# Optimization experiments

Hardware: AMD Instinct MI355X
Metric: run time of the kernel (lower is better)

## Reference

```python
import jax, jax.numpy as jnp
import numpy as np

EMBED = 2048
HEADS = 16
HEAD_DIM = EMBED // HEADS
CHUNK = 128
BASE = 10000.0
EPS = 1e-6


def setup_inputs() -> dict:
    key = jax.random.key(0)
    ks = jax.random.split(key, 8)
    b, n, d = 2, 2048, EMBED
    std = 0.02
    return {
        "x": jax.random.normal(ks[0], (b, n, d), jnp.float32),
        "Wq": jax.random.normal(ks[1], (d, d), jnp.float32) * std,
        "Wk": jax.random.normal(ks[2], (d, d), jnp.float32) * std,
        "Wv": jax.random.normal(ks[3], (d, d), jnp.float32) * std,
        "Wo": jax.random.normal(ks[4], (d, d), jnp.float32) * std,
        "Wg1": jax.random.normal(ks[5], (d, HEAD_DIM), jnp.float32) * std,
        "Wg2": jax.random.normal(ks[6], (HEAD_DIM, d), jnp.float32) * std,
        "norm_weight": jnp.ones((d,), jnp.float32),
    }


def _alibi_log_decay(h):
    # lightning attention 'constant' decay: per-head ALiBi slope, log_lambda = -slope
    slopes = 2.0 ** (-8.0 * (jnp.arange(h, dtype=jnp.float32) + 1.0) / h)
    return -slopes  # [h]


def _lrpe_rotate(x):
    # RoPE-like rotation on head_dim (half-split), offset=0
    b, n, h, d = x.shape
    half = d // 2
    theta = BASE ** (-2.0 * jnp.arange(half, dtype=jnp.float32) / d)  # [half]
    ang = jnp.arange(n, dtype=jnp.float32)[:, None] * theta[None, :]  # [n, half]
    cos = jnp.cos(ang)[None, :, None, :]
    sin = jnp.sin(ang)[None, :, None, :]
    x1, x2 = x[..., :half], x[..., half:]
    return jnp.concatenate([x1 * cos - x2 * sin, x1 * sin + x2 * cos], axis=-1)


def _lightning_attn(q, k, v, log_lam):
    # chunk-recurrent linear attention with per-head exponential decay
    b, n, h, d = q.shape
    C = CHUNK
    nc = n // C
    qc = q.reshape(b, nc, C, h, d).transpose(1, 0, 2, 3, 4)  # [nc,b,C,h,d]
    kc = k.reshape(b, nc, C, h, d).transpose(1, 0, 2, 3, 4)
    vc = v.reshape(b, nc, C, h, d).transpose(1, 0, 2, 3, 4)
    i = jnp.arange(C, dtype=jnp.float32)
    diff = i[:, None] - i[None, :]  # [C,C]
    # intra-chunk decay mask D[h,t,s] = lambda_h^(t-s) for t>=s else 0
    D = jnp.where(diff[None] >= 0, jnp.exp(log_lam[:, None, None] * diff[None]), 0.0)
    decay_q = jnp.exp(log_lam[None, :] * (i[:, None] + 1.0))    # [C,h]
    decay_k = jnp.exp(log_lam[None, :] * (C - 1.0 - i[:, None]))  # [C,h]
    lam_C = jnp.exp(log_lam * C)  # [h]

    def step(S, qkv):
        qi, ki, vi = qkv  # [b,C,h,d]
        scores = jnp.einsum('bthd,bshd->bhts', qi, ki) * D[None]
        o_intra = jnp.einsum('bhts,bshd->bthd', scores, vi)
        o_inter = jnp.einsum('bthd,bhde->bthe', qi * decay_q[None, :, :, None], S)
        S_new = lam_C[None, :, None, None] * S + jnp.einsum(
            'bshd,bshe->bhde', ki * decay_k[None, :, :, None], vi)
        return S_new, o_intra + o_inter

    S0 = jnp.zeros((b, h, d, d), q.dtype)
    _, o = jax.lax.scan(step, S0, (qc, kc, vc))  # o: [nc,b,C,h,d]
    return o.transpose(1, 0, 2, 3, 4).reshape(b, n, h, d)


def _gated_group_rmsnorm(o, gate, weight):
    # gate_pos='pre', gate_act='sigmoid', num_groups=HEADS
    b, n, d = o.shape
    x = o * jax.nn.sigmoid(gate)
    xg = x.reshape(b, n, HEADS, HEAD_DIM)
    ms = jnp.mean(xg * xg, axis=-1, keepdims=True)
    xg = xg * jax.lax.rsqrt(ms + EPS)
    return xg.reshape(b, n, d) * weight


def reference(x, Wq, Wk, Wv, Wo, Wg1, Wg2, norm_weight):
    b, n, d = x.shape
    q = (x @ Wq).reshape(b, n, HEADS, HEAD_DIM)
    k = (x @ Wk).reshape(b, n, HEADS, HEAD_DIM)
    v = (x @ Wv).reshape(b, n, HEADS, HEAD_DIM)
    q = jax.nn.silu(q)
    k = jax.nn.silu(k)
    q = _lrpe_rotate(q)
    k = _lrpe_rotate(k)
    log_lam = _alibi_log_decay(HEADS)
    o = _lightning_attn(q, k, v, log_lam).reshape(b, n, d)
    gate = (x @ Wg1) @ Wg2
    o = _gated_group_rmsnorm(o, gate, norm_weight)
    return o @ Wo
```

## Files before the change

kernel.cpp:

```cpp
#include <hip/hip_runtime.h>


#define DEV __device__ __forceinline__
typedef unsigned short u16;
typedef __bf16 bf16x8 __attribute__((ext_vector_type(8)));
typedef float f32x4 __attribute__((ext_vector_type(4)));
typedef u16 u16x8 __attribute__((ext_vector_type(8)));

DEV u16 f2bf(float f) {
  unsigned u = __builtin_bit_cast(unsigned, f);
  u += 0x7fffu + ((u >> 16) & 1u);
  return (u16)(u >> 16);
}
DEV float bf2f(u16 h) {
  unsigned u = ((unsigned)h) << 16;
  return __builtin_bit_cast(float, u);
}
DEV void async16(const u16* g, u16* l) {
  __builtin_amdgcn_global_load_lds(
      (const __attribute__((address_space(1))) unsigned int*)g,
      (__attribute__((address_space(3))) unsigned int*)l, 16, 0, 0);
}

__global__ void convert_f32_bf16(const float* __restrict__ in, u16* __restrict__ out, long n) {
  long i = ((long)blockIdx.x * blockDim.x + threadIdx.x) * 4;
  if (i >= n) return;
  float4 v = *(const float4*)(in + i);
  ushort4 p;
  p.x = f2bf(v.x); p.y = f2bf(v.y); p.z = f2bf(v.z); p.w = f2bf(v.w);
  *(ushort4*)(out + i) = p;
}

__global__ void transpose_all(const float* __restrict__ Wq, const float* __restrict__ Wk,
                              const float* __restrict__ Wv, const float* __restrict__ Wo,
                              const float* __restrict__ Wg1, const float* __restrict__ Wg2,
                              u16* __restrict__ wtqkv, u16* __restrict__ wot,
                              u16* __restrict__ wg1t, u16* __restrict__ wg2t) {
  __shared__ float t[32][33];
  int id = blockIdx.x;
  const float* in; u16* out; int K, N, bx, by;
  if (id < 12288) {
    int w = id >> 12, tt = id & 4095;
    in = (w == 0) ? Wq : (w == 1) ? Wk : Wv;
    out = wtqkv + (long)w * 2048 * 2048;
    K = 2048; N = 2048; bx = tt & 63; by = tt >> 6;
  } else if (id < 16384) {
    int tt = id - 12288;
    in = Wo; out = wot; K = 2048; N = 2048; bx = tt & 63; by = tt >> 6;
  } else if (id < 16640) {
    int tt = id - 16384;
    in = Wg1; out = wg1t; K = 2048; N = 128; bx = tt & 3; by = tt >> 2;
  } else {
    int tt = id - 16640;
    in = Wg2; out = wg2t; K = 128; N = 2048; bx = tt & 63; by = tt >> 6;
  }
  int c = threadIdx.x & 31, r0 = threadIdx.x >> 5;
  for (int r = r0; r < 32; r += 8)
    t[r][c] = in[(long)(by * 32 + r) * N + bx * 32 + c];
  __syncthreads();
  for (int r = r0; r < 32; r += 8)
    out[(long)(bx * 32 + r) * K + by * 32 + c] = f2bf(t[c][r]);
}

template <typename OutT>
__global__ __launch_bounds__(256, 2) void gemm_bt(
    const u16* __restrict__ A, const u16* __restrict__ B, OutT* __restrict__ C,
    int M, int N, int K, int lda, int ldb, int ldc,
    int nc, long sA1, long sA2, long sB1, long sB2, long sC1, long sC2) {
  __shared__ u16 sA[128 * 32], sB[128 * 32];
  {
    int z = blockIdx.z, z1 = z / nc, z2 = z % nc;
    A += z1 * sA1 + z2 * sA2;
    B += z1 * sB1 + z2 * sB2;
    C += z1 * sC1 + z2 * sC2;
  }
  const int tid = threadIdx.x, lane = tid & 63, wid = tid >> 6;
  const int bm = blockIdx.y * 128, bn = blockIdx.x * 128;
  const int ch0 = wid * 2, ch1 = ch0 + 1;
  const int lr = lane >> 2;
  const int ak = (((lane & 3) - ((lane >> 3) & 3)) & 3) * 8;
  const int ar0 = ch0 * 16 + lr, ar1 = ch1 * 16 + lr;
  const u16* gA0 = A + (long)(bm + ar0) * lda + ak;
  const u16* gA1 = A + (long)(bm + ar1) * lda + ak;
  const u16* gB0 = B + (long)(bn + ar0) * ldb + ak;
  const u16* gB1 = B + (long)(bn + ar1) * ldb + ak;
  u16* lA0 = sA + ch0 * 512; u16* lA1 = sA + ch1 * 512;
  u16* lB0 = sB + ch0 * 512; u16* lB1 = sB + ch1 * 512;
  const int wm = (wid & 1) * 64, wn = (wid >> 1) * 64;
  const int fm = lane & 15, kq = lane >> 4;
  const int qs = ((kq + (fm >> 1)) & 3) * 8;
  const int aoff = (wm >> 4) * 512 + fm * 32 + qs;
  const int boff = (wn >> 4) * 512 + fm * 32 + qs;
  f32x4 acc[4][4] = {};
  for (int kb = 0; kb < K; kb += 32) {
    async16(gA0, lA0); async16(gA1, lA1);
    async16(gB0, lB0); async16(gB1, lB1);
    gA0 += 32; gA1 += 32; gB0 += 32; gB1 += 32;
    __syncthreads();
    bf16x8 af[4], bfr[4];
#pragma unroll
    for (int i = 0; i < 4; i++) af[i] = *(const bf16x8*)&sA[aoff + i * 512];
#pragma unroll
    for (int i = 0; i < 4; i++) bfr[i] = *(const bf16x8*)&sB[boff + i * 512];
#pragma unroll
    for (int mt = 0; mt < 4; mt++)
#pragma unroll
      for (int nt = 0; nt < 4; nt++)
        acc[mt][nt] = __builtin_amdgcn_mfma_f32_16x16x32_bf16(af[mt], bfr[nt], acc[mt][nt], 0, 0, 0);
    __syncthreads();
  }
  const int cr = (lane >> 4) * 4;
#pragma unroll
  for (int mt = 0; mt < 4; mt++)
#pragma unroll
    for (int nt = 0; nt < 4; nt++)
#pragma unroll
      for (int r = 0; r < 4; r++) {
        long row = bm + wm + mt * 16 + cr + r;
        long col = bn + wn + nt * 16 + fm;
        float v = acc[mt][nt][r];
        if constexpr (sizeof(OutT) == 2) C[row * ldc + col] = f2bf(v);
        else                             C[row * ldc + col] = v;
      }
}

__global__ void reduce_g1(const float* __restrict__ p, u16* __restrict__ g1) {
  long i = ((long)blockIdx.x * 256 + threadIdx.x) * 4;
  float4 s = *(const float4*)(p + i);
#pragma unroll
  for (int z = 1; z < 8; z++) {
    float4 a = *(const float4*)(p + z * 524288L + i);
    s.x += a.x; s.y += a.y; s.z += a.z; s.w += a.w;
  }
  ushort4 o;
  o.x = f2bf(s.x); o.y = f2bf(s.y); o.z = f2bf(s.z); o.w = f2bf(s.w);
  *(ushort4*)(g1 + i) = o;
}

__global__ void silu_rotate(u16* __restrict__ qkv) {
  int idx = blockIdx.x * 256 + threadIdx.x;
  int j = idx & 63, h = (idx >> 6) & 15, t = (idx >> 10) & 2047, b = idx >> 21;
  u16* q = qkv + (long)(b * 2048 + t) * 6144 + h * 128;
  u16* k = q + 2048;
  float theta = exp2f(-13.287712379549449f * (float)j * (1.0f / 64.0f));
  float ang = (float)t * theta;
  float sn, cs;
  sincosf(ang, &sn, &cs);
  float q1 = bf2f(q[j]), q2 = bf2f(q[j + 64]);
  q1 = q1 / (1.f + expf(-q1)); q2 = q2 / (1.f + expf(-q2));
  q[j] = f2bf(q1 * cs - q2 * sn); q[j + 64] = f2bf(q1 * sn + q2 * cs);
  float k1 = bf2f(k[j]), k2 = bf2f(k[j + 64]);
  k1 = k1 / (1.f + expf(-k1)); k2 = k2 / (1.f + expf(-k2));
  k[j] = f2bf(k1 * cs - k2 * sn); k[j + 64] = f2bf(k1 * sn + k2 * cs);
}

__global__ void transpose_kv(const u16* __restrict__ qkv, u16* __restrict__ kdT,
                             u16* __restrict__ vT) {
  __shared__ float t[32][33];
  int z = blockIdx.z, which = z >> 5, bh = z & 31;
  int b = bh >> 4, h = bh & 15;
  u16* out = which ? vT : kdT;
  int slab = which ? 2 : 1, decay = which ? 0 : 1;
  int n0 = blockIdx.x * 32, d0 = blockIdx.y * 32;
  int cc = threadIdx.x & 31, rr0 = threadIdx.x >> 5;
  float log_lam = -exp2f(-0.5f * (float)(h + 1));
  for (int rr = rr0; rr < 32; rr += 8) {
    int n = n0 + rr;
    float v = bf2f(qkv[(long)(b * 2048 + n) * 6144 + slab * 2048 + h * 128 + d0 + cc]);
    if (decay) v *= expf(log_lam * (float)(127 - (n & 127)));
    t[rr][cc] = v;
  }
  __syncthreads();
  for (int rr = rr0; rr < 32; rr += 8)
    out[((long)bh * 128 + d0 + rr) * 2048 + n0 + cc] = f2bf(t[cc][rr]);
}

__global__ void scan_state(const u16* __restrict__ U, u16* __restrict__ S_all) {
  int blk = blockIdx.x;
  int bh = blk >> 3, sl = blk & 7, h = bh & 15;
  float log_lam = -exp2f(-0.5f * (float)(h + 1));
  float lamC = expf(log_lam * 128.f);
  long off = (long)bh * 16 * 16384 + sl * 2048 + threadIdx.x * 8;
  float s[8];
#pragma unroll
  for (int j = 0; j < 8; j++) s[j] = 0.f;
  for (int c = 0; c < 16; c++) {
    long idx = off + (long)c * 16384;
    u16x8 sb;
#pragma unroll
    for (int j = 0; j < 8; j++) sb[j] = f2bf(s[j]);
    *(u16x8*)(S_all + idx) = sb;
    u16x8 ub = *(const u16x8*)(U + idx);
#pragma unroll
    for (int j = 0; j < 8; j++) s[j] = lamC * s[j] + bf2f(ub[j]);
  }
}

__global__ __launch_bounds__(256, 1) void attn_out(
    const u16* __restrict__ qkv, const u16* __restrict__ vT,
    const u16* __restrict__ S_all, float* __restrict__ o) {
  __shared__ u16 sA[128 * 32], sB[128 * 32], sK[128 * 32];
  __shared__ u16 sS[128 * 136];
  const int blk = blockIdx.x;
  const int bh = blk >> 4, c = blk & 15;
  const int b = bh >> 4, h = bh & 15;
  const float log_lam = -exp2f(-0.5f * (float)(h + 1));
  const int tid = threadIdx.x, lane = tid & 63, wid = tid >> 6;
  const int wm = (wid & 1) * 64, wn = (wid >> 1) * 64;
  const int fm = lane & 15, fq = lane >> 4, kq = lane >> 4;
  const int ch0 = wid * 2, ch1 = ch0 + 1;
  const int lr = lane >> 2;
  const int ak = (((lane & 3) - ((lane >> 3) & 3)) & 3) * 8;
  const int r0 = ch0 * 16 + lr, r1 = ch1 * 16 + lr;
  const int qs = ((kq + (fm >> 1)) & 3) * 8;
  const int aoff = (wm >> 4) * 512 + fm * 32 + qs;
  const int boff = (wn >> 4) * 512 + fm * 32 + qs;
  const u16* qbase = qkv + (long)(b * 2048 + c * 128) * 6144 + h * 128;
  const u16* kbase = qbase + 2048;
  const u16* Sbase = S_all + ((long)bh * 16 + c) * 16384;
  const u16* vbase = vT + (long)bh * 262144 + (long)c * 128;

  f32x4 acc[4][4] = {};
  f32x4 sc[4][4] = {};
  for (int kb = 0; kb < 128; kb += 32) {
    async16(qbase + (long)r0 * 6144 + kb + ak, sA + ch0 * 512);
    async16(qbase + (long)r1 * 6144 + kb + ak, sA + ch1 * 512);
    async16(Sbase + r0 * 128 + kb + ak, sB + ch0 * 512);
    async16(Sbase + r1 * 128 + kb + ak, sB + ch1 * 512);
    async16(kbase + (long)r0 * 6144 + kb + ak, sK + ch0 * 512);
    async16(kbase + (long)r1 * 6144 + kb + ak, sK + ch1 * 512);
    __syncthreads();
    bf16x8 aq[4], bs[4], bk[4];
#pragma unroll
    for (int i = 0; i < 4; i++) {
      aq[i] = *(const bf16x8*)&sA[aoff + i * 512];
      bs[i] = *(const bf16x8*)&sB[boff + i * 512];
      bk[i] = *(const bf16x8*)&sK[boff + i * 512];
    }
#pragma unroll
    for (int mt = 0; mt < 4; mt++)
#pragma unroll
      for (int nt = 0; nt < 4; nt++) {
        acc[mt][nt] = __builtin_amdgcn_mfma_f32_16x16x32_bf16(aq[mt], bs[nt], acc[mt][nt], 0, 0, 0);
        sc[mt][nt] = __builtin_amdgcn_mfma_f32_16x16x32_bf16(aq[mt], bk[nt], sc[mt][nt], 0, 0, 0);
      }
    __syncthreads();
  }
#pragma unroll
  for (int mt = 0; mt < 4; mt++)
#pragma unroll
    for (int r = 0; r < 4; r++) {
      int t = wm + mt * 16 + fq * 4 + r;
      float d = expf(log_lam * (float)(t + 1));
#pragma unroll
      for (int nt = 0; nt < 4; nt++) acc[mt][nt][r] *= d;
    }
#pragma unroll
  for (int mt = 0; mt < 4; mt++)
#pragma unroll
    for (int nt = 0; nt < 4; nt++)
#pragma unroll
      for (int r = 0; r < 4; r++) {
        int t = wm + mt * 16 + fq * 4 + r;
        int s = wn + nt * 16 + fm;
        float v = sc[mt][nt][r];
        v = (t >= s) ? v * expf(log_lam * (float)(t - s)) : 0.f;
        sS[t * 136 + s] = f2bf(v);
      }
  __syncthreads();
  for (int kb = 0; kb < 128; kb += 32) {
    async16(vbase + r0 * 2048 + kb + ak, sB + ch0 * 512);
    async16(vbase + r1 * 2048 + kb + ak, sB + ch1 * 512);
    __syncthreads();
    bf16x8 as[4], bv[4];
#pragma unroll
    for (int i = 0; i < 4; i++) {
      as[i] = *(const bf16x8*)&sS[(wm + i * 16 + fm) * 136 + kb + kq * 8];
      bv[i] = *(const bf16x8*)&sB[boff + i * 512];
    }
#pragma unroll
    for (int mt = 0; mt < 4; mt++)
#pragma unroll
      for (int nt = 0; nt < 4; nt++)
        acc[mt][nt] = __builtin_amdgcn_mfma_f32_16x16x32_bf16(as[mt], bv[nt], acc[mt][nt], 0, 0, 0);
    __syncthreads();
  }
  long orow0 = (long)(b * 2048 + c * 128);
#pragma unroll
  for (int mt = 0; mt < 4; mt++)
#pragma unroll
    for (int nt = 0; nt < 4; nt++)
#pragma unroll
      for (int r = 0; r < 4; r++) {
        int t = wm + mt * 16 + fq * 4 + r;
        int e = wn + nt * 16 + fm;
        o[(orow0 + t) * 2048 + h * 128 + e] = acc[mt][nt][r];
      }
}

__global__ void gated_norm(const float* __restrict__ o, const u16* __restrict__ gate,
                           const float* __restrict__ w, u16* __restrict__ out) {
  int gidx = blockIdx.x * 4 + (threadIdx.x >> 6);
  int lane = threadIdx.x & 63;
  int h = gidx & 15;
  long base = (long)(gidx >> 4) * 2048 + h * 128;
  float x0 = o[base + lane], x1 = o[base + 64 + lane];
  float g0 = bf2f(gate[base + lane]), g1 = bf2f(gate[base + 64 + lane]);
  x0 *= 1.f / (1.f + expf(-g0));
  x1 *= 1.f / (1.f + expf(-g1));
  float ss = x0 * x0 + x1 * x1;
#pragma unroll
  for (int off = 32; off; off >>= 1) ss += __shfl_xor(ss, off);
  float r = rsqrtf(ss * (1.f / 128.f) + 1e-6f);
  out[base + lane] = f2bf(x0 * r * w[h * 128 + lane]);
  out[base + 64 + lane] = f2bf(x1 * r * w[h * 128 + 64 + lane]);
}

extern "C" void kernel_launch(void* const* d_in, const int* in_sizes, int n_in,
                              void* d_out, int out_size, void* d_ws, size_t ws_size,
                              hipStream_t stream) {
  (void)in_sizes; (void)n_in; (void)out_size; (void)ws_size;
  const float* x   = (const float*)d_in[0];
  const float* Wq  = (const float*)d_in[1];
  const float* Wk  = (const float*)d_in[2];
  const float* Wv  = (const float*)d_in[3];
  const float* Wo  = (const float*)d_in[4];
  const float* Wg1 = (const float*)d_in[5];
  const float* Wg2 = (const float*)d_in[6];
  const float* nw  = (const float*)d_in[7];
  float* out = (float*)d_out;

  char* ws = (char*)d_ws;
  size_t off = 0;
  auto alloc = [&](size_t bytes) -> void* {
    void* p = ws + off;
    off += (bytes + 255) & ~(size_t)255;
    return p;
  };
  u16* xb    = (u16*)alloc(4096UL * 2048 * 2);
  u16* wtqkv = (u16*)alloc(6144UL * 2048 * 2);
  u16* wot   = (u16*)alloc(2048UL * 2048 * 2);
  u16* wg1t  = (u16*)alloc(128UL * 2048 * 2);
  u16* wg2t  = (u16*)alloc(2048UL * 128 * 2);
  u16* qkv   = (u16*)alloc(4096UL * 6144 * 2);
  u16* g1    = (u16*)alloc(4096UL * 128 * 2);
  u16* gate  = (u16*)alloc(4096UL * 2048 * 2);
  u16* kdT   = (u16*)alloc(32UL * 128 * 2048 * 2);
  u16* vT    = (u16*)alloc(32UL * 128 * 2048 * 2);
  u16* Ubuf  = (u16*)alloc(512UL * 16384 * 2);
  u16* S_all = (u16*)alloc(512UL * 16384 * 2);
  float* ob  = (float*)alloc(4096UL * 2048 * 4);
  u16* nrm   = (u16*)alloc(4096UL * 2048 * 2);
  float* g1p = (float*)gate;

  convert_f32_bf16<<<dim3(8192), dim3(256), 0, stream>>>(x, xb, 8388608L);
  transpose_all<<<dim3(16896), dim3(256), 0, stream>>>(Wq, Wk, Wv, Wo, Wg1, Wg2,
                                                       wtqkv, wot, wg1t, wg2t);
  gemm_bt<u16><<<dim3(48, 32, 1), dim3(256), 0, stream>>>(xb, wtqkv, qkv,
      4096, 6144, 2048, 2048, 2048, 6144, 1, 0, 0, 0, 0, 0, 0);
  gemm_bt<float><<<dim3(1, 32, 8), dim3(256), 0, stream>>>(xb, wg1t, g1p,
      4096, 128, 256, 2048, 2048, 128, 1, 256L, 0, 256L, 0, 524288L, 0);
  silu_rotate<<<dim3(16384), dim3(256), 0, stream>>>(qkv);
  reduce_g1<<<dim3(512), dim3(256), 0, stream>>>(g1p, g1);
  gemm_bt<u16><<<dim3(16, 32, 1), dim3(256), 0, stream>>>(g1, wg2t, gate,
      4096, 2048, 128, 128, 128, 2048, 1, 0, 0, 0, 0, 0, 0);
  transpose_kv<<<dim3(64, 4, 64), dim3(256), 0, stream>>>(qkv, kdT, vT);
  gemm_bt<u16><<<dim3(1, 1, 512), dim3(256), 0, stream>>>(vT, kdT, Ubuf,
      128, 128, 128, 2048, 2048, 128,
      16, 262144L, 128L, 262144L, 128L, 262144L, 16384L);
  scan_state<<<dim3(256), dim3(256), 0, stream>>>(Ubuf, S_all);
  attn_out<<<dim3(512), dim3(256), 0, stream>>>(qkv, vT, S_all, ob);
  gated_norm<<<dim3(16384), dim3(256), 0, stream>>>(ob, gate, nw, nrm);
  gemm_bt<float><<<dim3(16, 32, 1), dim3(256), 0, stream>>>(nrm, wot, out,
      4096, 2048, 2048, 2048, 2048, 2048, 1, 0, 0, 0, 0, 0, 0);
}
```

Measured before the change: 449.3 us.

## Fuse gate projection, SiLU-rotate, and gated norm into GEMM epilogues

Appends Wg1 to the QKV weight so one GEMM also produces the low-rank gate input, removing the split-K gate GEMM and its reduction. SiLU plus the rotary rotation now run in the QKV GEMM epilogue, using a column permutation of Wq/Wk so each lane holds paired halves. The sigmoid gate and group RMSNorm move into the attn_out epilogue, which drops the fp32 intermediate and the separate norm kernel. GEMM blocks are also remapped in groups of 16 columns for L2 reuse; the cost is heavier epilogues with scattered 2-byte stores and an extra padded column tile.

```diff
diff --git a/kernel.cpp b/kernel.cpp
--- a/kernel.cpp
+++ b/kernel.cpp
@@ -34,22 +34,24 @@
 __global__ void transpose_all(const float* __restrict__ Wq, const float* __restrict__ Wk,
                               const float* __restrict__ Wv, const float* __restrict__ Wo,
                               const float* __restrict__ Wg1, const float* __restrict__ Wg2,
-                              u16* __restrict__ wtqkv, u16* __restrict__ wot,
-                              u16* __restrict__ wg1t, u16* __restrict__ wg2t) {
+                              u16* __restrict__ wtqkvg, u16* __restrict__ wot,
+                              u16* __restrict__ wg2t) {
   __shared__ float t[32][33];
   int id = blockIdx.x;
   const float* in; u16* out; int K, N, bx, by;
+  bool perm = false;
   if (id < 12288) {
     int w = id >> 12, tt = id & 4095;
     in = (w == 0) ? Wq : (w == 1) ? Wk : Wv;
-    out = wtqkv + (long)w * 2048 * 2048;
+    out = wtqkvg + (long)w * 2048 * 2048;
     K = 2048; N = 2048; bx = tt & 63; by = tt >> 6;
+    perm = (w < 2);
   } else if (id < 16384) {
     int tt = id - 12288;
     in = Wo; out = wot; K = 2048; N = 2048; bx = tt & 63; by = tt >> 6;
   } else if (id < 16640) {
     int tt = id - 16384;
-    in = Wg1; out = wg1t; K = 2048; N = 128; bx = tt & 3; by = tt >> 2;
+    in = Wg1; out = wtqkvg + 6144L * 2048; K = 2048; N = 128; bx = tt & 3; by = tt >> 2;
   } else {
     int tt = id - 16640;
     in = Wg2; out = wg2t; K = 128; N = 2048; bx = tt & 63; by = tt >> 6;
@@ -58,14 +60,20 @@
   for (int r = r0; r < 32; r += 8)
     t[r][c] = in[(long)(by * 32 + r) * N + bx * 32 + c];
   __syncthreads();
-  for (int r = r0; r < 32; r += 8)
-    out[(long)(bx * 32 + r) * K + by * 32 + c] = f2bf(t[c][r]);
+  for (int r = r0; r < 32; r += 8) {
+    int n = bx * 32 + r, nr = n;
+    if (perm) {
+      int h = n >> 7, j = n & 127, jj = j & 63, hi = j >> 6;
+      nr = h * 128 + (jj & 15) + 32 * (jj >> 4) + 16 * hi;
+    }
+    out[(long)nr * K + by * 32 + c] = f2bf(t[c][r]);
+  }
 }
 
 template <typename OutT>
 __global__ __launch_bounds__(256, 2) void gemm_bt(
     const u16* __restrict__ A, const u16* __restrict__ B, OutT* __restrict__ C,
-    int M, int N, int K, int lda, int ldb, int ldc,
+    int M, int N, int K, int lda, int ldb, int ldc, int rot,
     int nc, long sA1, long sA2, long sB1, long sB2, long sC1, long sC2) {
   __shared__ u16 sA[128 * 32], sB[128 * 32];
   {
@@ -74,8 +82,17 @@
     B += z1 * sB1 + z2 * sB2;
     C += z1 * sC1 + z2 * sC2;
   }
+  int bxs, bys;
+  {
+    int lin = blockIdx.x + gridDim.x * blockIdx.y;
+    int per = 16 * gridDim.y;
+    int g = lin / per, r = lin % per;
+    int base = g * 16;
+    int w = min(16, (int)gridDim.x - base);
+    bxs = base + r % w; bys = r / w;
+  }
   const int tid = threadIdx.x, lane = tid & 63, wid = tid >> 6;
-  const int bm = blockIdx.y * 128, bn = blockIdx.x * 128;
+  const int bm = bys * 128, bn = bxs * 128;
   const int ch0 = wid * 2, ch1 = ch0 + 1;
   const int lr = lane >> 2;
   const int ak = (((lane & 3) - ((lane >> 3) & 3)) & 3) * 8;
@@ -110,6 +127,30 @@
     __syncthreads();
   }
   const int cr = (lane >> 4) * 4;
+  if constexpr (sizeof(OutT) == 2) {
+    if (rot && bn < 4096) {
+#pragma unroll
+      for (int mt = 0; mt < 4; mt++)
+#pragma unroll
+        for (int r = 0; r < 4; r++) {
+          long row = bm + wm + mt * 16 + cr + r;
+          float tf = (float)(int)(row & 2047);
+#pragma unroll
+          for (int np = 0; np < 4; np += 2) {
+            float x1 = acc[mt][np][r], x2 = acc[mt][np + 1][r];
+            x1 = x1 / (1.f + __expf(-x1));
+            x2 = x2 / (1.f + __expf(-x2));
+            int jj = fm + 16 * ((wn >> 5) + (np >> 1));
+            float th = exp2f(-13.287712379549449f * (float)jj * (1.f / 64.f));
+            float sn, cs;
+            sincosf(tf * th, &sn, &cs);
+            C[row * ldc + bn + jj]      = f2bf(x1 * cs - x2 * sn);
+            C[row * ldc + bn + 64 + jj] = f2bf(x1 * sn + x2 * cs);
+          }
+        }
+      return;
+    }
+  }
 #pragma unroll
   for (int mt = 0; mt < 4; mt++)
 #pragma unroll
@@ -122,36 +163,6 @@
         if constexpr (sizeof(OutT) == 2) C[row * ldc + col] = f2bf(v);
         else                             C[row * ldc + col] = v;
       }
-}
-
-__global__ void reduce_g1(const float* __restrict__ p, u16* __restrict__ g1) {
-  long i = ((long)blockIdx.x * 256 + threadIdx.x) * 4;
-  float4 s = *(const float4*)(p + i);
-#pragma unroll
-  for (int z = 1; z < 8; z++) {
-    float4 a = *(const float4*)(p + z * 524288L + i);
-    s.x += a.x; s.y += a.y; s.z += a.z; s.w += a.w;
-  }
-  ushort4 o;
-  o.x = f2bf(s.x); o.y = f2bf(s.y); o.z = f2bf(s.z); o.w = f2bf(s.w);
-  *(ushort4*)(g1 + i) = o;
-}
-
-__global__ void silu_rotate(u16* __restrict__ qkv) {
-  int idx = blockIdx.x * 256 + threadIdx.x;
-  int j = idx & 63, h = (idx >> 6) & 15, t = (idx >> 10) & 2047, b = idx >> 21;
-  u16* q = qkv + (long)(b * 2048 + t) * 6144 + h * 128;
-  u16* k = q + 2048;
-  float theta = exp2f(-13.287712379549449f * (float)j * (1.0f / 64.0f));
-  float ang = (float)t * theta;
-  float sn, cs;
-  sincosf(ang, &sn, &cs);
-  float q1 = bf2f(q[j]), q2 = bf2f(q[j + 64]);
-  q1 = q1 / (1.f + expf(-q1)); q2 = q2 / (1.f + expf(-q2));
-  q[j] = f2bf(q1 * cs - q2 * sn); q[j + 64] = f2bf(q1 * sn + q2 * cs);
-  float k1 = bf2f(k[j]), k2 = bf2f(k[j + 64]);
-  k1 = k1 / (1.f + expf(-k1)); k2 = k2 / (1.f + expf(-k2));
-  k[j] = f2bf(k1 * cs - k2 * sn); k[j + 64] = f2bf(k1 * sn + k2 * cs);
 }
 
 __global__ void transpose_kv(const u16* __restrict__ qkv, u16* __restrict__ kdT,
@@ -166,7 +177,7 @@
   float log_lam = -exp2f(-0.5f * (float)(h + 1));
   for (int rr = rr0; rr < 32; rr += 8) {
     int n = n0 + rr;
-    float v = bf2f(qkv[(long)(b * 2048 + n) * 6144 + slab * 2048 + h * 128 + d0 + cc]);
+    float v = bf2f(qkv[(long)(b * 2048 + n) * 6272 + slab * 2048 + h * 128 + d0 + cc]);
     if (decay) v *= expf(log_lam * (float)(127 - (n & 127)));
     t[rr][cc] = v;
   }
@@ -198,9 +209,11 @@
 
 __global__ __launch_bounds__(256, 1) void attn_out(
     const u16* __restrict__ qkv, const u16* __restrict__ vT,
-    const u16* __restrict__ S_all, float* __restrict__ o) {
+    const u16* __restrict__ S_all, const u16* __restrict__ gate,
+    const float* __restrict__ nw, u16* __restrict__ nrm) {
   __shared__ u16 sA[128 * 32], sB[128 * 32], sK[128 * 32];
   __shared__ u16 sS[128 * 136];
+  __shared__ float sNorm[2][128];
   const int blk = blockIdx.x;
   const int bh = blk >> 4, c = blk & 15;
   const int b = bh >> 4, h = bh & 15;
@@ -208,14 +221,14 @@
   const int tid = threadIdx.x, lane = tid & 63, wid = tid >> 6;
   const int wm = (wid & 1) * 64, wn = (wid >> 1) * 64;
   const int fm = lane & 15, fq = lane >> 4, kq = lane >> 4;
-  const int ch0 = wid * 2, ch1 = ch0 + 1;
   const int lr = lane >> 2;
   const int ak = (((lane & 3) - ((lane >> 3) & 3)) & 3) * 8;
+  const int ch0 = wid * 2, ch1 = ch0 + 1;
   const int r0 = ch0 * 16 + lr, r1 = ch1 * 16 + lr;
   const int qs = ((kq + (fm >> 1)) & 3) * 8;
   const int aoff = (wm >> 4) * 512 + fm * 32 + qs;
   const int boff = (wn >> 4) * 512 + fm * 32 + qs;
-  const u16* qbase = qkv + (long)(b * 2048 + c * 128) * 6144 + h * 128;
+  const u16* qbase = qkv + (long)(b * 2048 + c * 128) * 6272 + h * 128;
   const u16* kbase = qbase + 2048;
   const u16* Sbase = S_all + ((long)bh * 16 + c) * 16384;
   const u16* vbase = vT + (long)bh * 262144 + (long)c * 128;
@@ -223,12 +236,12 @@
   f32x4 acc[4][4] = {};
   f32x4 sc[4][4] = {};
   for (int kb = 0; kb < 128; kb += 32) {
-    async16(qbase + (long)r0 * 6144 + kb + ak, sA + ch0 * 512);
-    async16(qbase + (long)r1 * 6144 + kb + ak, sA + ch1 * 512);
+    async16(qbase + (long)r0 * 6272 + kb + ak, sA + ch0 * 512);
+    async16(qbase + (long)r1 * 6272 + kb + ak, sA + ch1 * 512);
     async16(Sbase + r0 * 128 + kb + ak, sB + ch0 * 512);
     async16(Sbase + r1 * 128 + kb + ak, sB + ch1 * 512);
-    async16(kbase + (long)r0 * 6144 + kb + ak, sK + ch0 * 512);
-    async16(kbase + (long)r1 * 6144 + kb + ak, sK + ch1 * 512);
+    async16(kbase + (long)r0 * 6272 + kb + ak, sK + ch0 * 512);
+    async16(kbase + (long)r1 * 6272 + kb + ak, sK + ch1 * 512);
     __syncthreads();
     bf16x8 aq[4], bs[4], bk[4];
 #pragma unroll
@@ -285,35 +298,55 @@
         acc[mt][nt] = __builtin_amdgcn_mfma_f32_16x16x32_bf16(as[mt], bv[nt], acc[mt][nt], 0, 0, 0);
     __syncthreads();
   }
+  const u16* gbase = gate + (long)(b * 2048 + c * 128) * 2048 + h * 128;
+  float nwv[4];
+#pragma unroll
+  for (int nt = 0; nt < 4; nt++) nwv[nt] = nw[h * 128 + wn + nt * 16 + fm];
+  float part[4][4];
+#pragma unroll
+  for (int mt = 0; mt < 4; mt++)
+#pragma unroll
+    for (int r = 0; r < 4; r++) {
+      int t = wm + mt * 16 + fq * 4 + r;
+      float p = 0.f;
+#pragma unroll
+      for (int nt = 0; nt < 4; nt++) {
+        int e = wn + nt * 16 + fm;
+        float g = bf2f(gbase[(long)t * 2048 + e]);
+        float x = acc[mt][nt][r] / (1.f + __expf(-g));
+        acc[mt][nt][r] = x;
+        p += x * x;
+      }
+      part[mt][r] = p;
+    }
+#pragma unroll
+  for (int o = 1; o < 16; o <<= 1)
+#pragma unroll
+    for (int mt = 0; mt < 4; mt++)
+#pragma unroll
+      for (int r = 0; r < 4; r++) part[mt][r] += __shfl_xor(part[mt][r], o);
+  if (fm == 0) {
+#pragma unroll
+    for (int mt = 0; mt < 4; mt++)
+#pragma unroll
+      for (int r = 0; r < 4; r++)
+        sNorm[wid >> 1][wm + mt * 16 + fq * 4 + r] = part[mt][r];
+  }
+  __syncthreads();
   long orow0 = (long)(b * 2048 + c * 128);
 #pragma unroll
   for (int mt = 0; mt < 4; mt++)
 #pragma unroll
-    for (int nt = 0; nt < 4; nt++)
-#pragma unroll
-      for (int r = 0; r < 4; r++) {
-        int t = wm + mt * 16 + fq * 4 + r;
+    for (int r = 0; r < 4; r++) {
+      int t = wm + mt * 16 + fq * 4 + r;
+      float ms = (sNorm[0][t] + sNorm[1][t]) * (1.f / 128.f);
+      float rs = rsqrtf(ms + 1e-6f);
+#pragma unroll
+      for (int nt = 0; nt < 4; nt++) {
         int e = wn + nt * 16 + fm;
-        o[(orow0 + t) * 2048 + h * 128 + e] = acc[mt][nt][r];
+        nrm[(orow0 + t) * 2048 + h * 128 + e] = f2bf(acc[mt][nt][r] * rs * nwv[nt]);
       }
-}
-
-__global__ void gated_norm(const float* __restrict__ o, const u16* __restrict__ gate,
-                           const float* __restrict__ w, u16* __restrict__ out) {
-  int gidx = blockIdx.x * 4 + (threadIdx.x >> 6);
-  int lane = threadIdx.x & 63;
-  int h = gidx & 15;
-  long base = (long)(gidx >> 4) * 2048 + h * 128;
-  float x0 = o[base + lane], x1 = o[base + 64 + lane];
-  float g0 = bf2f(gate[base + lane]), g1 = bf2f(gate[base + 64 + lane]);
-  x0 *= 1.f / (1.f + expf(-g0));
-  x1 *= 1.f / (1.f + expf(-g1));
-  float ss = x0 * x0 + x1 * x1;
-#pragma unroll
-  for (int off = 32; off; off >>= 1) ss += __shfl_xor(ss, off);
-  float r = rsqrtf(ss * (1.f / 128.f) + 1e-6f);
-  out[base + lane] = f2bf(x0 * r * w[h * 128 + lane]);
-  out[base + 64 + lane] = f2bf(x1 * r * w[h * 128 + 64 + lane]);
+    }
 }
 
 extern "C" void kernel_launch(void* const* d_in, const int* in_sizes, int n_in,
@@ -338,39 +371,30 @@
     return p;
   };
   u16* xb    = (u16*)alloc(4096UL * 2048 * 2);
-  u16* wtqkv = (u16*)alloc(6144UL * 2048 * 2);
+  u16* wtqkv = (u16*)alloc(6272UL * 2048 * 2);
   u16* wot   = (u16*)alloc(2048UL * 2048 * 2);
-  u16* wg1t  = (u16*)alloc(128UL * 2048 * 2);
   u16* wg2t  = (u16*)alloc(2048UL * 128 * 2);
-  u16* qkv   = (u16*)alloc(4096UL * 6144 * 2);
-  u16* g1    = (u16*)alloc(4096UL * 128 * 2);
+  u16* qkvg  = (u16*)alloc(4096UL * 6272 * 2);
   u16* gate  = (u16*)alloc(4096UL * 2048 * 2);
   u16* kdT   = (u16*)alloc(32UL * 128 * 2048 * 2);
   u16* vT    = (u16*)alloc(32UL * 128 * 2048 * 2);
   u16* Ubuf  = (u16*)alloc(512UL * 16384 * 2);
   u16* S_all = (u16*)alloc(512UL * 16384 * 2);
-  float* ob  = (float*)alloc(4096UL * 2048 * 4);
   u16* nrm   = (u16*)alloc(4096UL * 2048 * 2);
-  float* g1p = (float*)gate;
 
   convert_f32_bf16<<<dim3(8192), dim3(256), 0, stream>>>(x, xb, 8388608L);
   transpose_all<<<dim3(16896), dim3(256), 0, stream>>>(Wq, Wk, Wv, Wo, Wg1, Wg2,
-                                                       wtqkv, wot, wg1t, wg2t);
-  gemm_bt<u16><<<dim3(48, 32, 1), dim3(256), 0, stream>>>(xb, wtqkv, qkv,
-      4096, 6144, 2048, 2048, 2048, 6144, 1, 0, 0, 0, 0, 0, 0);
-  gemm_bt<float><<<dim3(1, 32, 8), dim3(256), 0, stream>>>(xb, wg1t, g1p,
-      4096, 128, 256, 2048, 2048, 128, 1, 256L, 0, 256L, 0, 524288L, 0);
-  silu_rotate<<<dim3(16384), dim3(256), 0, stream>>>(qkv);
-  reduce_g1<<<dim3(512), dim3(256), 0, stream>>>(g1p, g1);
-  gemm_bt<u16><<<dim3(16, 32, 1), dim3(256), 0, stream>>>(g1, wg2t, gate,
-      4096, 2048, 128, 128, 128, 2048, 1, 0, 0, 0, 0, 0, 0);
-  transpose_kv<<<dim3(64, 4, 64), dim3(256), 0, stream>>>(qkv, kdT, vT);
+                                                       wtqkv, wot, wg2t);
+  gemm_bt<u16><<<dim3(49, 32, 1), dim3(256), 0, stream>>>(xb, wtqkv, qkvg,
+      4096, 6272, 2048, 2048, 2048, 6272, 1, 1, 0, 0, 0, 0, 0, 0);
+  gemm_bt<u16><<<dim3(16, 32, 1), dim3(256), 0, stream>>>(qkvg + 6144, wg2t, gate,
+      4096, 2048, 128, 6272, 128, 2048, 0, 1, 0, 0, 0, 0, 0, 0);
+  transpose_kv<<<dim3(64, 4, 64), dim3(256), 0, stream>>>(qkvg, kdT, vT);
   gemm_bt<u16><<<dim3(1, 1, 512), dim3(256), 0, stream>>>(vT, kdT, Ubuf,
-      128, 128, 128, 2048, 2048, 128,
+      128, 128, 128, 2048, 2048, 128, 0,
       16, 262144L, 128L, 262144L, 128L, 262144L, 16384L);
   scan_state<<<dim3(256), dim3(256), 0, stream>>>(Ubuf, S_all);
-  attn_out<<<dim3(512), dim3(256), 0, stream>>>(qkv, vT, S_all, ob);
-  gated_norm<<<dim3(16384), dim3(256), 0, stream>>>(ob, gate, nw, nrm);
+  attn_out<<<dim3(512), dim3(256), 0, stream>>>(qkvg, vT, S_all, gate, nw, nrm);
   gemm_bt<float><<<dim3(16, 32, 1), dim3(256), 0, stream>>>(nrm, wot, out,
-      4096, 2048, 2048, 2048, 2048, 2048, 1, 0, 0, 0, 0, 0, 0);
-}
+      4096, 2048, 2048, 2048, 2048, 2048, 0, 1, 0, 0, 0, 0, 0, 0);
+}
```

Measured after the change: 424.5 us. 1.06x faster.
